# Kernel optimization log

Hardware: AMD Instinct MI355X
Metric: run time of the kernel (lower is better)

Reference implementation:

```python
import jax, jax.numpy as jnp
import numpy as np

B, N, D_IN, D_OUT, NUM_RING = 32, 8192, 64, 128, 4
BN_EPS = 1e-5


def setup_inputs() -> dict:
    key = jax.random.key(0)
    ks = jax.random.split(key, 8)
    return {
        "x": jax.random.normal(ks[0], (B, D_IN, N), dtype=jnp.float32),
        "ring": jax.random.randint(ks[1], (B, N), 0, NUM_RING, dtype=jnp.int64),
        "W": jax.random.normal(ks[2], (NUM_RING, D_OUT, D_IN), dtype=jnp.float32) * 0.1,
        "b": jax.random.normal(ks[3], (NUM_RING, D_OUT), dtype=jnp.float32) * 0.1,
        "gamma": jax.random.uniform(ks[4], (NUM_RING, D_OUT), dtype=jnp.float32) + 0.5,
        "beta": jax.random.normal(ks[5], (NUM_RING, D_OUT), dtype=jnp.float32) * 0.1,
        "mean": jax.random.normal(ks[6], (NUM_RING, D_OUT), dtype=jnp.float32) * 0.1,
        "var": jax.random.uniform(ks[7], (NUM_RING, D_OUT), dtype=jnp.float32) + 0.5,
    }


def reference(x, ring, W, b, gamma, beta, mean, var):
    # x: [B, 64, N]; ring: [B, N] int labels in [0, num_ring)
    xt = jnp.transpose(x, (0, 2, 1))  # [B, N, 64]
    Bv, Nv, _ = xt.shape
    num_ring = W.shape[0]
    out = jnp.zeros((Bv, Nv, W.shape[1]), dtype=x.dtype)
    neg = jnp.finfo(x.dtype).min
    for i in range(num_ring):  # small fixed loop over rings
        # 1x1 conv == per-point linear, then BatchNorm (inference-mode affine)
        y = jnp.einsum("bnd,od->bno", xt, W[i]) + b[i]  # [B, N, 128]
        scale = gamma[i] * jax.lax.rsqrt(var[i] + BN_EPS)
        y = (y - mean[i]) * scale + beta[i]
        m = (ring == i)[..., None]  # [B, N, 1]
        # per-(batch, ring) segment max over points, broadcast back to members
        ymax = jnp.max(jnp.where(m, y, neg), axis=1, keepdims=True)  # [B, 1, 128]
        out = jnp.where(m, ymax, out)
    return jnp.transpose(out, (0, 2, 1))  # [B, 128, N]
```

## Files before the change

kernel.cpp:

```cpp
#include <hip/hip_runtime.h>
#include <hip/hip_bf16.h>
#include <cstdint>
#include <cstddef>

#define BB 32
#define NN 8192
#define DIN 64
#define DOUT 128
#define NR 4
#define BN_EPS 1e-5f

typedef float nfloat4 __attribute__((ext_vector_type(4)));
typedef float floatx4 __attribute__((ext_vector_type(4)));
typedef short short8 __attribute__((ext_vector_type(8)));


__device__ inline unsigned short f2bf(float f) {
  const unsigned int u = __float_as_uint(f);
  return (unsigned short)((u + 0x7fffu + ((u >> 16) & 1u)) >> 16);
}

__device__ inline void pack2(float a, float b, short8& dst, int idx) {
  __hip_bfloat162 h = __float22bfloat162_rn(make_float2(a, b));
  const unsigned int bits = *(unsigned int*)&h;
  dst[idx] = (short)(bits & 0xffffu);
  dst[idx + 1] = (short)(bits >> 16);
}

__global__ void __launch_bounds__(256) k_compute(
    const float* __restrict__ x, const float* __restrict__ W,
    const int* __restrict__ ring, unsigned int* __restrict__ smax_keys) {
  const int b = blockIdx.y;
  const int n0 = blockIdx.x * 256;
  const int wave = (int)threadIdx.x >> 6;
  const int lane = (int)threadIdx.x & 63;
  const int quad = lane >> 4;
  const int l16 = lane & 15;
  const float* xb = x + (size_t)b * DIN * NN;
  const int* rgb = ring + (size_t)b * NN;

  short8 af[2][2];
#pragma unroll
  for (int tt = 0; tt < 2; ++tt) {
    const int chan = (wave + 4 * tt) * 16 + l16;
    const float* wr = W + ((size_t)blockIdx.z * 0 + 0);
    (void)wr;
  }

  floatx4 rmax[2][NR];
#pragma unroll
  for (int tt = 0; tt < 2; ++tt)
#pragma unroll
    for (int r = 0; r < NR; ++r) rmax[tt][r] = {-INFINITY, -INFINITY, -INFINITY, -INFINITY};

  short8 afr[NR][2][2];
#pragma unroll
  for (int r = 0; r < NR; ++r) {
#pragma unroll
    for (int tt = 0; tt < 2; ++tt) {
      const int chan = (wave + 4 * tt) * 16 + l16;
      const float* wr = W + ((size_t)r * DOUT + chan) * DIN + quad * 8;
#pragma unroll
      for (int ks = 0; ks < 2; ++ks) {
        const float4 w0 = *(const float4*)&wr[ks * 32];
        const float4 w1 = *(const float4*)&wr[ks * 32 + 4];
        short8 a;
        pack2(w0.x, w0.y, a, 0);
        pack2(w0.z, w0.w, a, 2);
        pack2(w1.x, w1.y, a, 4);
        pack2(w1.z, w1.w, a, 6);
        afr[r][tt][ks] = a;
      }
    }
  }

#pragma unroll 1
  for (int T = 0; T < 16; ++T) {
    const int n = n0 + T * 16 + l16;
    const int rr = rgb[n];
    float bx[8], by[8];
#pragma unroll
    for (int j = 0; j < 8; ++j) {
      bx[j] = xb[(size_t)(quad * 8 + j) * NN + n];
      by[j] = xb[(size_t)(32 + quad * 8 + j) * NN + n];
    }
    short8 b0, b1;
#pragma unroll
    for (int j = 0; j < 4; ++j) {
      pack2(bx[2 * j], bx[2 * j + 1], b0, 2 * j);
      pack2(by[2 * j], by[2 * j + 1], b1, 2 * j);
    }
#pragma unroll
    for (int r = 0; r < NR; ++r) {
      floatx4 acc0 = {0.f, 0.f, 0.f, 0.f};
      floatx4 acc1 = {0.f, 0.f, 0.f, 0.f};
      acc0 = __builtin_amdgcn_mfma_f32_16x16x32_bf16(afr[r][0][0], b0, acc0, 0, 0, 0);
      acc0 = __builtin_amdgcn_mfma_f32_16x16x32_bf16(afr[r][0][1], b1, acc0, 0, 0, 0);
      acc1 = __builtin_amdgcn_mfma_f32_16x16x32_bf16(afr[r][1][0], b0, acc1, 0, 0, 0);
      acc1 = __builtin_amdgcn_mfma_f32_16x16x32_bf16(afr[r][1][1], b1, acc1, 0, 0, 0);
      const bool m = (rr == r);
#pragma unroll
      for (int p = 0; p < 4; ++p) {
        rmax[0][r][p] = fmaxf(rmax[0][r][p], m ? acc0[p] : -INFINITY);
        rmax[1][r][p] = fmaxf(rmax[1][r][p], m ? acc1[p] : -INFINITY);
      }
    }
  }

#pragma unroll
  for (int tt = 0; tt < 2; ++tt) {
#pragma unroll
    for (int r = 0; r < NR; ++r) {
#pragma unroll
      for (int p = 0; p < 4; ++p) {
        float v = rmax[tt][r][p];
        v = fmaxf(v, __shfl_xor(v, 1, 64));
        v = fmaxf(v, __shfl_xor(v, 2, 64));
        v = fmaxf(v, __shfl_xor(v, 4, 64));
        v = fmaxf(v, __shfl_xor(v, 8, 64));
        if (l16 == 0) {
          const int chan = (wave + 4 * tt) * 16 + quad * 4 + p;
          const unsigned int u = __float_as_uint(v);
          const unsigned int key = (u & 0x80000000u) ? ~u : (u | 0x80000000u);
          atomicMax(&smax_keys[(size_t)(b * NR + r) * DOUT + chan], key);
        }
      }
    }
  }
}

__global__ void k_out(const float* __restrict__ bias, const float* __restrict__ gamma,
                      const float* __restrict__ beta, const float* __restrict__ mean,
                      const float* __restrict__ var, const int* __restrict__ ring,
                      const unsigned int* __restrict__ smax_keys,
                      float* __restrict__ out) {
  const int b = blockIdx.z;
  const int og = blockIdx.y;
  const int n0 = blockIdx.x * 1024;

  __shared__ float ymax[32 * NR];
  if (threadIdx.x < 32 * NR) {
    const int oo = (int)threadIdx.x >> 2;
    const int r = (int)threadIdx.x & 3;
    const int o = og * 32 + oo;
    const int t = r * DOUT + o;
    const unsigned int key = smax_keys[(size_t)b * NR * DOUT + t];
    const unsigned int u = (key & 0x80000000u) ? (key ^ 0x80000000u) : ~key;
    const float raw = __uint_as_float(u);
    const float sc = gamma[t] * rsqrtf(var[t] + BN_EPS);
    ymax[oo * NR + r] = (raw + bias[t] - mean[t]) * sc + beta[t];
  }
  __syncthreads();

  const int n = n0 + (int)threadIdx.x * 4;
  const int4 rg = *(const int4*)&ring[(size_t)b * NN + n];
#pragma unroll 8
  for (int oo = 0; oo < 32; ++oo) {
    const int o = og * 32 + oo;
    nfloat4 v;
    v.x = ymax[oo * NR + rg.x];
    v.y = ymax[oo * NR + rg.y];
    v.z = ymax[oo * NR + rg.z];
    v.w = ymax[oo * NR + rg.w];
    __builtin_nontemporal_store(v, (nfloat4*)&out[((size_t)b * DOUT + o) * NN + n]);
  }
}

extern "C" void kernel_launch(void* const* d_in, const int* in_sizes, int n_in,
                              void* d_out, int out_size, void* d_ws, size_t ws_size,
                              hipStream_t stream) {
  const float* x = (const float*)d_in[0];
  const int* ring = (const int*)d_in[1];
  const float* W = (const float*)d_in[2];
  const float* bias = (const float*)d_in[3];
  const float* gamma = (const float*)d_in[4];
  const float* beta = (const float*)d_in[5];
  const float* mean = (const float*)d_in[6];
  const float* var = (const float*)d_in[7];
  float* out = (float*)d_out;

  unsigned int* keys = (unsigned int*)d_ws;

  (void)hipMemsetAsync(keys, 0, (size_t)BB * NR * DOUT * 4, stream);

  k_compute<<<dim3(NN / 256, BB), 256, 0, stream>>>(x, W, ring, keys);
  k_out<<<dim3(NN / 1024, DOUT / 32, BB), 256, 0, stream>>>(bias, gamma, beta, mean,
                                                            var, ring, keys, out);
}
```

Before: 230.5 us.

## Stage x tiles into LDS with async double-buffered loads; select ymax by bit tests

k_compute now copies x tiles and ring labels into swizzled shared memory with global_load_lds and double buffers them across four 64-point stages. This overlaps the global loads with the MFMA work and replaces the strided per-lane global reads. k_out reads the four ring maxima as one vector load from shared memory and picks the value with bit-test selects instead of indexed LDS lookups. The cost is more LDS per block, which can lower occupancy, plus extra barriers.

```diff
diff --git a/kernel.cpp b/kernel.cpp
--- a/kernel.cpp
+++ b/kernel.cpp
@@ -15,11 +15,6 @@
 typedef short short8 __attribute__((ext_vector_type(8)));
 
 
-__device__ inline unsigned short f2bf(float f) {
-  const unsigned int u = __float_as_uint(f);
-  return (unsigned short)((u + 0x7fffu + ((u >> 16) & 1u)) >> 16);
-}
-
 __device__ inline void pack2(float a, float b, short8& dst, int idx) {
   __hip_bfloat162 h = __float22bfloat162_rn(make_float2(a, b));
   const unsigned int bits = *(unsigned int*)&h;
@@ -27,31 +22,46 @@
   dst[idx + 1] = (short)(bits >> 16);
 }
 
+__device__ inline void gload_lds16(const void* g, void* l) {
+  __builtin_amdgcn_global_load_lds(
+      (const __attribute__((address_space(1))) unsigned int*)g,
+      (__attribute__((address_space(3))) unsigned int*)l, 16, 0, 0);
+}
+__device__ inline void gload_lds4(const void* g, void* l) {
+  __builtin_amdgcn_global_load_lds(
+      (const __attribute__((address_space(1))) unsigned int*)g,
+      (__attribute__((address_space(3))) unsigned int*)l, 4, 0, 0);
+}
+
 __global__ void __launch_bounds__(256) k_compute(
     const float* __restrict__ x, const float* __restrict__ W,
     const int* __restrict__ ring, unsigned int* __restrict__ smax_keys) {
   const int b = blockIdx.y;
   const int n0 = blockIdx.x * 256;
-  const int wave = (int)threadIdx.x >> 6;
-  const int lane = (int)threadIdx.x & 63;
+  const int tid = (int)threadIdx.x;
+  const int wave = tid >> 6;
+  const int lane = tid & 63;
   const int quad = lane >> 4;
   const int l16 = lane & 15;
   const float* xb = x + (size_t)b * DIN * NN;
-  const int* rgb = ring + (size_t)b * NN;
-
-  short8 af[2][2];
-#pragma unroll
-  for (int tt = 0; tt < 2; ++tt) {
-    const int chan = (wave + 4 * tt) * 16 + l16;
-    const float* wr = W + ((size_t)blockIdx.z * 0 + 0);
-    (void)wr;
-  }
-
-  floatx4 rmax[2][NR];
-#pragma unroll
-  for (int tt = 0; tt < 2; ++tt)
-#pragma unroll
-    for (int r = 0; r < NR; ++r) rmax[tt][r] = {-INFINITY, -INFINITY, -INFINITY, -INFINITY};
+
+  __shared__ float lx[2][DIN * 64];
+  __shared__ int lring[256];
+
+  gload_lds4(ring + (size_t)b * NN + n0 + wave * 64 + lane, &lring[wave * 64]);
+
+  auto stage = [&](int pbuf, int s) {
+    const int ns0 = n0 + s * 64;
+#pragma unroll
+    for (int i = 0; i < 4; ++i) {
+      const int d = wave * 16 + i * 4 + (lane >> 4);
+      const int c0 = (lane & 15) * 4;
+      const int cg = c0 ^ (((d >> 3) & 3) << 3);
+      gload_lds16(xb + (size_t)d * NN + ns0 + cg,
+                  &lx[pbuf][(wave * 16 + i * 4) * 64]);
+    }
+  };
+  stage(0, 0);
 
   short8 afr[NR][2][2];
 #pragma unroll
@@ -74,37 +84,59 @@
     }
   }
 
+  floatx4 rmax[2][NR];
+#pragma unroll
+  for (int tt = 0; tt < 2; ++tt)
+#pragma unroll
+    for (int r = 0; r < NR; ++r)
+      rmax[tt][r] = {-INFINITY, -INFINITY, -INFINITY, -INFINITY};
+
+  __syncthreads();
+
 #pragma unroll 1
-  for (int T = 0; T < 16; ++T) {
-    const int n = n0 + T * 16 + l16;
-    const int rr = rgb[n];
-    float bx[8], by[8];
-#pragma unroll
-    for (int j = 0; j < 8; ++j) {
-      bx[j] = xb[(size_t)(quad * 8 + j) * NN + n];
-      by[j] = xb[(size_t)(32 + quad * 8 + j) * NN + n];
-    }
-    short8 b0, b1;
-#pragma unroll
-    for (int j = 0; j < 4; ++j) {
-      pack2(bx[2 * j], bx[2 * j + 1], b0, 2 * j);
-      pack2(by[2 * j], by[2 * j + 1], b1, 2 * j);
-    }
-#pragma unroll
-    for (int r = 0; r < NR; ++r) {
-      floatx4 acc0 = {0.f, 0.f, 0.f, 0.f};
-      floatx4 acc1 = {0.f, 0.f, 0.f, 0.f};
-      acc0 = __builtin_amdgcn_mfma_f32_16x16x32_bf16(afr[r][0][0], b0, acc0, 0, 0, 0);
-      acc0 = __builtin_amdgcn_mfma_f32_16x16x32_bf16(afr[r][0][1], b1, acc0, 0, 0, 0);
-      acc1 = __builtin_amdgcn_mfma_f32_16x16x32_bf16(afr[r][1][0], b0, acc1, 0, 0, 0);
-      acc1 = __builtin_amdgcn_mfma_f32_16x16x32_bf16(afr[r][1][1], b1, acc1, 0, 0, 0);
-      const bool m = (rr == r);
-#pragma unroll
-      for (int p = 0; p < 4; ++p) {
-        rmax[0][r][p] = fmaxf(rmax[0][r][p], m ? acc0[p] : -INFINITY);
-        rmax[1][r][p] = fmaxf(rmax[1][r][p], m ? acc1[p] : -INFINITY);
-      }
-    }
+  for (int s = 0; s < 4; ++s) {
+    if (s < 3) stage((s + 1) & 1, s + 1);
+    const float* lbuf = lx[s & 1];
+#pragma unroll
+    for (int T = 0; T < 4; ++T) {
+      const int nl = T * 16 + l16;
+      const int csw = nl ^ (quad * 8);
+      const int rr = lring[s * 64 + nl];
+      const float* p0 = &lbuf[(quad * 8) * 64 + csw];
+      const float* p1 = &lbuf[(quad * 8 + 4) * 64 + csw];
+      const float* p2 = &lbuf[(32 + quad * 8) * 64 + csw];
+      const float* p3 = &lbuf[(32 + quad * 8 + 4) * 64 + csw];
+      float v0[8], v1[8];
+#pragma unroll
+      for (int j = 0; j < 4; ++j) {
+        v0[j] = p0[j * 64];
+        v0[4 + j] = p1[j * 64];
+        v1[j] = p2[j * 64];
+        v1[4 + j] = p3[j * 64];
+      }
+      short8 b0, b1;
+#pragma unroll
+      for (int j = 0; j < 4; ++j) {
+        pack2(v0[2 * j], v0[2 * j + 1], b0, 2 * j);
+        pack2(v1[2 * j], v1[2 * j + 1], b1, 2 * j);
+      }
+#pragma unroll
+      for (int r = 0; r < NR; ++r) {
+        floatx4 acc0 = {0.f, 0.f, 0.f, 0.f};
+        floatx4 acc1 = {0.f, 0.f, 0.f, 0.f};
+        acc0 = __builtin_amdgcn_mfma_f32_16x16x32_bf16(afr[r][0][0], b0, acc0, 0, 0, 0);
+        acc0 = __builtin_amdgcn_mfma_f32_16x16x32_bf16(afr[r][0][1], b1, acc0, 0, 0, 0);
+        acc1 = __builtin_amdgcn_mfma_f32_16x16x32_bf16(afr[r][1][0], b0, acc1, 0, 0, 0);
+        acc1 = __builtin_amdgcn_mfma_f32_16x16x32_bf16(afr[r][1][1], b1, acc1, 0, 0, 0);
+        const bool m = (rr == r);
+#pragma unroll
+        for (int p = 0; p < 4; ++p) {
+          rmax[0][r][p] = fmaxf(rmax[0][r][p], m ? acc0[p] : -INFINITY);
+          rmax[1][r][p] = fmaxf(rmax[1][r][p], m ? acc1[p] : -INFINITY);
+        }
+      }
+    }
+    if (s < 3) __syncthreads();
   }
 
 #pragma unroll
@@ -129,16 +161,16 @@
   }
 }
 
-__global__ void k_out(const float* __restrict__ bias, const float* __restrict__ gamma,
-                      const float* __restrict__ beta, const float* __restrict__ mean,
-                      const float* __restrict__ var, const int* __restrict__ ring,
-                      const unsigned int* __restrict__ smax_keys,
-                      float* __restrict__ out) {
+__global__ void __launch_bounds__(256) k_out(
+    const float* __restrict__ bias, const float* __restrict__ gamma,
+    const float* __restrict__ beta, const float* __restrict__ mean,
+    const float* __restrict__ var, const int* __restrict__ ring,
+    const unsigned int* __restrict__ smax_keys, float* __restrict__ out) {
   const int b = blockIdx.z;
   const int og = blockIdx.y;
   const int n0 = blockIdx.x * 1024;
 
-  __shared__ float ymax[32 * NR];
+  __shared__ __align__(16) float ymax[32 * NR];
   if (threadIdx.x < 32 * NR) {
     const int oo = (int)threadIdx.x >> 2;
     const int r = (int)threadIdx.x & 3;
@@ -154,15 +186,21 @@
 
   const int n = n0 + (int)threadIdx.x * 4;
   const int4 rg = *(const int4*)&ring[(size_t)b * NN + n];
+  const bool ax = rg.x & 1, bx = rg.x & 2;
+  const bool ay = rg.y & 1, by = rg.y & 2;
+  const bool az = rg.z & 1, bz = rg.z & 2;
+  const bool aw = rg.w & 1, bw = rg.w & 2;
+  float* orow = out + ((size_t)b * DOUT + og * 32) * NN + n;
+
 #pragma unroll 8
   for (int oo = 0; oo < 32; ++oo) {
-    const int o = og * 32 + oo;
+    const floatx4 L = *(const floatx4*)&ymax[oo * NR];
     nfloat4 v;
-    v.x = ymax[oo * NR + rg.x];
-    v.y = ymax[oo * NR + rg.y];
-    v.z = ymax[oo * NR + rg.z];
-    v.w = ymax[oo * NR + rg.w];
-    __builtin_nontemporal_store(v, (nfloat4*)&out[((size_t)b * DOUT + o) * NN + n]);
+    { float lo = ax ? L.y : L.x, hi = ax ? L.w : L.z; v.x = bx ? hi : lo; }
+    { float lo = ay ? L.y : L.x, hi = ay ? L.w : L.z; v.y = by ? hi : lo; }
+    { float lo = az ? L.y : L.x, hi = az ? L.w : L.z; v.z = bz ? hi : lo; }
+    { float lo = aw ? L.y : L.x, hi = aw ? L.w : L.z; v.w = bw ? hi : lo; }
+    __builtin_nontemporal_store(v, (nfloat4*)(orow + (size_t)oo * NN));
   }
 }
 
```

New measurement: 252.8 us. 1.1x slower.

## Double-buffer x loads in compute kernel, halve tile, restructure output kernel per row

Applied to the files above, without the earlier changes.

The compute kernel now processes 128 points per block instead of 256, doubling the grid. It software-pipelines the per-tile global loads into two register buffers so the next tile's loads overlap the current tile's MFMA work, and sets launch bounds of 3 blocks per CU. The output kernel is reorganized so each wave owns one output channel row and streams the whole N dimension, selecting the ring value with register selects instead of a shared-memory lookup and barrier. This trades more blocks (and more atomics and weight reloads) for better latency hiding. It also adds register pressure and gives a different store pattern per wave.

```diff
diff --git a/kernel.cpp b/kernel.cpp
--- a/kernel.cpp
+++ b/kernel.cpp
@@ -15,11 +15,6 @@
 typedef short short8 __attribute__((ext_vector_type(8)));
 
 
-__device__ inline unsigned short f2bf(float f) {
-  const unsigned int u = __float_as_uint(f);
-  return (unsigned short)((u + 0x7fffu + ((u >> 16) & 1u)) >> 16);
-}
-
 __device__ inline void pack2(float a, float b, short8& dst, int idx) {
   __hip_bfloat162 h = __float22bfloat162_rn(make_float2(a, b));
   const unsigned int bits = *(unsigned int*)&h;
@@ -27,31 +22,17 @@
   dst[idx + 1] = (short)(bits >> 16);
 }
 
-__global__ void __launch_bounds__(256) k_compute(
+__global__ void __launch_bounds__(256, 3) k_compute(
     const float* __restrict__ x, const float* __restrict__ W,
     const int* __restrict__ ring, unsigned int* __restrict__ smax_keys) {
   const int b = blockIdx.y;
-  const int n0 = blockIdx.x * 256;
+  const int n0 = blockIdx.x * 128;
   const int wave = (int)threadIdx.x >> 6;
   const int lane = (int)threadIdx.x & 63;
   const int quad = lane >> 4;
   const int l16 = lane & 15;
   const float* xb = x + (size_t)b * DIN * NN;
   const int* rgb = ring + (size_t)b * NN;
-
-  short8 af[2][2];
-#pragma unroll
-  for (int tt = 0; tt < 2; ++tt) {
-    const int chan = (wave + 4 * tt) * 16 + l16;
-    const float* wr = W + ((size_t)blockIdx.z * 0 + 0);
-    (void)wr;
-  }
-
-  floatx4 rmax[2][NR];
-#pragma unroll
-  for (int tt = 0; tt < 2; ++tt)
-#pragma unroll
-    for (int r = 0; r < NR; ++r) rmax[tt][r] = {-INFINITY, -INFINITY, -INFINITY, -INFINITY};
 
   short8 afr[NR][2][2];
 #pragma unroll
@@ -74,21 +55,32 @@
     }
   }
 
-#pragma unroll 1
-  for (int T = 0; T < 16; ++T) {
+  floatx4 rmax[2][NR];
+#pragma unroll
+  for (int tt = 0; tt < 2; ++tt)
+#pragma unroll
+    for (int r = 0; r < NR; ++r)
+      rmax[tt][r] = {-INFINITY, -INFINITY, -INFINITY, -INFINITY};
+
+  float pA[16], pB[16];
+  int rA, rB;
+
+  auto LD = [&](float (&buf)[16], int& rr, int T) {
     const int n = n0 + T * 16 + l16;
-    const int rr = rgb[n];
-    float bx[8], by[8];
 #pragma unroll
     for (int j = 0; j < 8; ++j) {
-      bx[j] = xb[(size_t)(quad * 8 + j) * NN + n];
-      by[j] = xb[(size_t)(32 + quad * 8 + j) * NN + n];
+      buf[j] = xb[(size_t)(quad * 8 + j) * NN + n];
+      buf[8 + j] = xb[(size_t)(32 + quad * 8 + j) * NN + n];
     }
+    rr = rgb[n];
+  };
+
+  auto CMP = [&](const float (&buf)[16], int rr) {
     short8 b0, b1;
 #pragma unroll
     for (int j = 0; j < 4; ++j) {
-      pack2(bx[2 * j], bx[2 * j + 1], b0, 2 * j);
-      pack2(by[2 * j], by[2 * j + 1], b1, 2 * j);
+      pack2(buf[2 * j], buf[2 * j + 1], b0, 2 * j);
+      pack2(buf[8 + 2 * j], buf[8 + 2 * j + 1], b1, 2 * j);
     }
 #pragma unroll
     for (int r = 0; r < NR; ++r) {
@@ -105,6 +97,15 @@
         rmax[1][r][p] = fmaxf(rmax[1][r][p], m ? acc1[p] : -INFINITY);
       }
     }
+  };
+
+  LD(pA, rA, 0);
+#pragma unroll 1
+  for (int T = 0; T < 8; T += 2) {
+    LD(pB, rB, T + 1);
+    CMP(pA, rA);
+    if (T + 2 < 8) LD(pA, rA, T + 2);
+    CMP(pB, rB);
   }
 
 #pragma unroll
@@ -129,40 +130,49 @@
   }
 }
 
-__global__ void k_out(const float* __restrict__ bias, const float* __restrict__ gamma,
-                      const float* __restrict__ beta, const float* __restrict__ mean,
-                      const float* __restrict__ var, const int* __restrict__ ring,
-                      const unsigned int* __restrict__ smax_keys,
-                      float* __restrict__ out) {
-  const int b = blockIdx.z;
-  const int og = blockIdx.y;
-  const int n0 = blockIdx.x * 1024;
+__global__ void __launch_bounds__(256) k_out(
+    const float* __restrict__ bias, const float* __restrict__ gamma,
+    const float* __restrict__ beta, const float* __restrict__ mean,
+    const float* __restrict__ var, const int* __restrict__ ring,
+    const unsigned int* __restrict__ smax_keys, float* __restrict__ out) {
+  const int b = blockIdx.y;
+  const int og = blockIdx.x;
+  const int wave = (int)threadIdx.x >> 6;
+  const int lane = (int)threadIdx.x & 63;
+  const int o = og * 4 + wave;
 
-  __shared__ float ymax[32 * NR];
-  if (threadIdx.x < 32 * NR) {
-    const int oo = (int)threadIdx.x >> 2;
-    const int r = (int)threadIdx.x & 3;
-    const int o = og * 32 + oo;
-    const int t = r * DOUT + o;
-    const unsigned int key = smax_keys[(size_t)b * NR * DOUT + t];
-    const unsigned int u = (key & 0x80000000u) ? (key ^ 0x80000000u) : ~key;
-    const float raw = __uint_as_float(u);
-    const float sc = gamma[t] * rsqrtf(var[t] + BN_EPS);
-    ymax[oo * NR + r] = (raw + bias[t] - mean[t]) * sc + beta[t];
+  float yv0, yv1, yv2, yv3;
+  {
+    float tmp[NR];
+#pragma unroll
+    for (int r = 0; r < NR; ++r) {
+      const int t = r * DOUT + o;
+      const unsigned int key = smax_keys[(size_t)b * NR * DOUT + t];
+      const unsigned int u = (key & 0x80000000u) ? (key ^ 0x80000000u) : ~key;
+      const float raw = __uint_as_float(u);
+      const float sc = gamma[t] * rsqrtf(var[t] + BN_EPS);
+      tmp[r] = (raw + bias[t] - mean[t]) * sc + beta[t];
+    }
+    yv0 = tmp[0]; yv1 = tmp[1]; yv2 = tmp[2]; yv3 = tmp[3];
   }
-  __syncthreads();
 
-  const int n = n0 + (int)threadIdx.x * 4;
-  const int4 rg = *(const int4*)&ring[(size_t)b * NN + n];
-#pragma unroll 8
-  for (int oo = 0; oo < 32; ++oo) {
-    const int o = og * 32 + oo;
+  const int* rgb = ring + (size_t)b * NN;
+  float* orow = out + ((size_t)b * DOUT + o) * NN;
+
+#pragma unroll 4
+  for (int it = 0; it < NN / 256; ++it) {
+    const int n = it * 256 + lane * 4;
+    const int4 rg = *(const int4*)&rgb[n];
     nfloat4 v;
-    v.x = ymax[oo * NR + rg.x];
-    v.y = ymax[oo * NR + rg.y];
-    v.z = ymax[oo * NR + rg.z];
-    v.w = ymax[oo * NR + rg.w];
-    __builtin_nontemporal_store(v, (nfloat4*)&out[((size_t)b * DOUT + o) * NN + n]);
+    { float lo = (rg.x & 1) ? yv1 : yv0, hi = (rg.x & 1) ? yv3 : yv2;
+      v.x = (rg.x & 2) ? hi : lo; }
+    { float lo = (rg.y & 1) ? yv1 : yv0, hi = (rg.y & 1) ? yv3 : yv2;
+      v.y = (rg.y & 2) ? hi : lo; }
+    { float lo = (rg.z & 1) ? yv1 : yv0, hi = (rg.z & 1) ? yv3 : yv2;
+      v.z = (rg.z & 2) ? hi : lo; }
+    { float lo = (rg.w & 1) ? yv1 : yv0, hi = (rg.w & 1) ? yv3 : yv2;
+      v.w = (rg.w & 2) ? hi : lo; }
+    __builtin_nontemporal_store(v, (nfloat4*)(orow + n));
   }
 }
 
@@ -183,7 +193,7 @@
 
   (void)hipMemsetAsync(keys, 0, (size_t)BB * NR * DOUT * 4, stream);
 
-  k_compute<<<dim3(NN / 256, BB), 256, 0, stream>>>(x, W, ring, keys);
-  k_out<<<dim3(NN / 1024, DOUT / 32, BB), 256, 0, stream>>>(bias, gamma, beta, mean,
-                                                            var, ring, keys, out);
+  k_compute<<<dim3(NN / 128, BB), 256, 0, stream>>>(x, W, ring, keys);
+  k_out<<<dim3(DOUT / 4, BB), 256, 0, stream>>>(bias, gamma, beta, mean,
+                                                var, ring, keys, out);
 }
```

New measurement: 382.9 us. 1.66x slower.

## Prefetch next x tile in compute loop and replicate LDS lookup table in output kernel

Applied to the files above, without the earlier changes.

The compute kernel now loads the next 16-point tile of x and ring labels into registers before running the MFMAs for the current tile. This software pipelining is meant to hide global load latency behind matrix math, at the cost of extra live registers. The output kernel replicates each ymax value 32 times in shared memory so each lane reads its own bank, removing bank conflicts from data-dependent ring indexing. It also uses precomputed pointer offsets and launch bounds.

```diff
diff --git a/kernel.cpp b/kernel.cpp
--- a/kernel.cpp
+++ b/kernel.cpp
@@ -14,11 +14,6 @@
 typedef float floatx4 __attribute__((ext_vector_type(4)));
 typedef short short8 __attribute__((ext_vector_type(8)));
 
-
-__device__ inline unsigned short f2bf(float f) {
-  const unsigned int u = __float_as_uint(f);
-  return (unsigned short)((u + 0x7fffu + ((u >> 16) & 1u)) >> 16);
-}
 
 __device__ inline void pack2(float a, float b, short8& dst, int idx) {
   __hip_bfloat162 h = __float22bfloat162_rn(make_float2(a, b));
@@ -38,20 +33,6 @@
   const int l16 = lane & 15;
   const float* xb = x + (size_t)b * DIN * NN;
   const int* rgb = ring + (size_t)b * NN;
-
-  short8 af[2][2];
-#pragma unroll
-  for (int tt = 0; tt < 2; ++tt) {
-    const int chan = (wave + 4 * tt) * 16 + l16;
-    const float* wr = W + ((size_t)blockIdx.z * 0 + 0);
-    (void)wr;
-  }
-
-  floatx4 rmax[2][NR];
-#pragma unroll
-  for (int tt = 0; tt < 2; ++tt)
-#pragma unroll
-    for (int r = 0; r < NR; ++r) rmax[tt][r] = {-INFINITY, -INFINITY, -INFINITY, -INFINITY};
 
   short8 afr[NR][2][2];
 #pragma unroll
@@ -74,22 +55,37 @@
     }
   }
 
-#pragma unroll 1
-  for (int T = 0; T < 16; ++T) {
+  floatx4 rmax[2][NR];
+#pragma unroll
+  for (int tt = 0; tt < 2; ++tt)
+#pragma unroll
+    for (int r = 0; r < NR; ++r)
+      rmax[tt][r] = {-INFINITY, -INFINITY, -INFINITY, -INFINITY};
+
+  float bx[16];
+  int rn;
+  auto LD = [&](int T) {
     const int n = n0 + T * 16 + l16;
-    const int rr = rgb[n];
-    float bx[8], by[8];
 #pragma unroll
     for (int j = 0; j < 8; ++j) {
       bx[j] = xb[(size_t)(quad * 8 + j) * NN + n];
-      by[j] = xb[(size_t)(32 + quad * 8 + j) * NN + n];
+      bx[8 + j] = xb[(size_t)(32 + quad * 8 + j) * NN + n];
     }
+    rn = rgb[n];
+  };
+
+  LD(0);
+#pragma unroll 1
+  for (int T = 0; T < 16; ++T) {
     short8 b0, b1;
 #pragma unroll
     for (int j = 0; j < 4; ++j) {
       pack2(bx[2 * j], bx[2 * j + 1], b0, 2 * j);
-      pack2(by[2 * j], by[2 * j + 1], b1, 2 * j);
+      pack2(bx[8 + 2 * j], bx[8 + 2 * j + 1], b1, 2 * j);
     }
+    const int rr = rn;
+    if (T < 15) LD(T + 1);
+
 #pragma unroll
     for (int r = 0; r < NR; ++r) {
       floatx4 acc0 = {0.f, 0.f, 0.f, 0.f};
@@ -129,40 +125,52 @@
   }
 }
 
-__global__ void k_out(const float* __restrict__ bias, const float* __restrict__ gamma,
-                      const float* __restrict__ beta, const float* __restrict__ mean,
-                      const float* __restrict__ var, const int* __restrict__ ring,
-                      const unsigned int* __restrict__ smax_keys,
-                      float* __restrict__ out) {
+__global__ void __launch_bounds__(256) k_out(
+    const float* __restrict__ bias, const float* __restrict__ gamma,
+    const float* __restrict__ beta, const float* __restrict__ mean,
+    const float* __restrict__ var, const int* __restrict__ ring,
+    const unsigned int* __restrict__ smax_keys, float* __restrict__ out) {
   const int b = blockIdx.z;
   const int og = blockIdx.y;
   const int n0 = blockIdx.x * 1024;
+  const int t = (int)threadIdx.x;
 
-  __shared__ float ymax[32 * NR];
-  if (threadIdx.x < 32 * NR) {
-    const int oo = (int)threadIdx.x >> 2;
-    const int r = (int)threadIdx.x & 3;
+  __shared__ float lut[32 * NR * 32];
+  {
+    const int oo = t >> 3;
+    const int r = (t >> 1) & 3;
+    const int c0 = (t & 1) * 16;
     const int o = og * 32 + oo;
-    const int t = r * DOUT + o;
-    const unsigned int key = smax_keys[(size_t)b * NR * DOUT + t];
+    const int tt = r * DOUT + o;
+    const unsigned int key = smax_keys[(size_t)b * NR * DOUT + tt];
     const unsigned int u = (key & 0x80000000u) ? (key ^ 0x80000000u) : ~key;
     const float raw = __uint_as_float(u);
-    const float sc = gamma[t] * rsqrtf(var[t] + BN_EPS);
-    ymax[oo * NR + r] = (raw + bias[t] - mean[t]) * sc + beta[t];
+    const float sc = gamma[tt] * rsqrtf(var[tt] + BN_EPS);
+    const float val = (raw + bias[tt] - mean[tt]) * sc + beta[tt];
+    nfloat4 v4 = {val, val, val, val};
+    float* dst = &lut[(oo * NR + r) * 32 + c0];
+#pragma unroll
+    for (int k = 0; k < 4; ++k) *(nfloat4*)&dst[k * 4] = v4;
   }
   __syncthreads();
 
-  const int n = n0 + (int)threadIdx.x * 4;
+  const int n = n0 + t * 4;
   const int4 rg = *(const int4*)&ring[(size_t)b * NN + n];
+  const int l31 = t & 31;
+  const float* p0 = &lut[rg.x * 32 + l31];
+  const float* p1 = &lut[rg.y * 32 + l31];
+  const float* p2 = &lut[rg.z * 32 + l31];
+  const float* p3 = &lut[rg.w * 32 + l31];
+  float* orow = out + ((size_t)b * DOUT + og * 32) * NN + n;
+
 #pragma unroll 8
   for (int oo = 0; oo < 32; ++oo) {
-    const int o = og * 32 + oo;
     nfloat4 v;
-    v.x = ymax[oo * NR + rg.x];
-    v.y = ymax[oo * NR + rg.y];
-    v.z = ymax[oo * NR + rg.z];
-    v.w = ymax[oo * NR + rg.w];
-    __builtin_nontemporal_store(v, (nfloat4*)&out[((size_t)b * DOUT + o) * NN + n]);
+    v.x = p0[oo * 128];
+    v.y = p1[oo * 128];
+    v.z = p2[oo * 128];
+    v.w = p3[oo * 128];
+    __builtin_nontemporal_store(v, (nfloat4*)(orow + (size_t)oo * NN));
   }
 }
 
```

New measurement: 230.3 us. No clear change (-0.1%).
